# Kernel tuning notes

Measured on AMD Instinct MI355X. Metric: run time of the kernel, lower is better.

The kernel has to match this reference:

```python
import jax, jax.numpy as jnp
import numpy as np

HEAD_DIM = 128
NUM_Q_HEAD = 32
NUM_KV_HEAD = 8
WINDOW = 512
CAUSAL = True
SCALE = 1.0 / float(np.sqrt(HEAD_DIM))  # softmax_scale default 1/sqrt(d)
CAP = 30.0                               # softmax capping (temp ignored when cap is set)
CLIP_LO, CLIP_HI = -0.01, 1.01           # softmax clip range
NEG_INF = -1e30


def setup_inputs() -> dict:
    key = jax.random.key(0)
    kq, kk, kv = jax.random.split(key, 3)
    B, SQ, SK = 2, 2048, 2048
    q = jax.random.normal(kq, (B, SQ, NUM_Q_HEAD, HEAD_DIM), dtype=jnp.float32)
    k = jax.random.normal(kk, (B, SK, NUM_KV_HEAD, HEAD_DIM), dtype=jnp.float32)
    v = jax.random.normal(kv, (B, SK, NUM_KV_HEAD, HEAD_DIM), dtype=jnp.float32)
    return {"q": q, "k": k, "v": v}


def _sliding_window_mask(sq, sk):
    # query position i attends to kv position j with bottom-right alignment
    i = jnp.arange(sq)[:, None] + (sk - sq)  # [sq, 1]
    j = jnp.arange(sk)[None, :]              # [1, sk]
    allowed = j >= (i - WINDOW)
    if CAUSAL:
        allowed = allowed & (j <= i)
    else:
        allowed = allowed & (j <= i + WINDOW)
    return allowed  # [sq, sk] bool


def _attn(q, k, v):
    # q: [b, sq, hq, d]; k, v: [b, sk, hkv, d]
    B, SQ, HQ, D = q.shape
    SK = k.shape[1]
    groups = HQ // k.shape[2]
    k = jnp.repeat(k, groups, axis=2)  # GQA expand -> [b, sk, hq, d]
    v = jnp.repeat(v, groups, axis=2)

    logits = jnp.einsum('bqhd,bkhd->bhqk', q, k) * SCALE
    logits = CAP * jnp.tanh(logits / CAP)  # softmax capping

    allowed = _sliding_window_mask(SQ, SK)  # [sq, sk]
    logits = jnp.where(allowed[None, None], logits, NEG_INF)

    p = jax.nn.softmax(logits, axis=-1)
    # softmax clipping: clamp((hi-lo)*p + lo, 0, 1)
    p = jnp.clip((CLIP_HI - CLIP_LO) * p + CLIP_LO, 0.0, 1.0)

    out = jnp.einsum('bhqk,bkhd->bqhd', p, v)
    # rows with no allowed kv position -> zero output (torch code zeroes NaN rows)
    row_ok = jnp.any(allowed, axis=-1)  # [sq]
    out = jnp.where(row_ok[None, :, None, None], out, 0.0)
    return out


def reference(q, k, v):
    return _attn(q, k, v)
```

## Files before the change

### kernel.cpp

```cpp
#include <hip/hip_runtime.h>
#include <hip/hip_bf16.h>

#define B_    2
#define SQ_   2048
#define SK_   2048
#define HQ_   32
#define HKV_  8
#define D_    128
#define W_    512
#define KVT   64
#define MAXT  9

typedef short s16x8 __attribute__((ext_vector_type(8)));
typedef float f32x4 __attribute__((ext_vector_type(4)));

static __device__ __forceinline__ short bf16b(float x){
    __hip_bfloat16 h = __float2bfloat16(x);
    return *reinterpret_cast<short*>(&h);
}
static __device__ __forceinline__ float b2f(short u){
    return __uint_as_float(((unsigned)(unsigned short)u) << 16);
}
static __device__ __forceinline__ float fexp2(float x){ return __builtin_amdgcn_exp2f(x); }
static __device__ __forceinline__ unsigned pk2(float a, float b){
    return ((unsigned)(unsigned short)bf16b(a)) | (((unsigned)(unsigned short)bf16b(b)) << 16);
}

__global__ __launch_bounds__(512)
void attn_kernel(const float* __restrict__ q, const float* __restrict__ k,
                 const float* __restrict__ v, float* __restrict__ out){
    __shared__ short KV[KVT * D_];
    __shared__ short Pb[8 * 16 * KVT];

    int bid = blockIdx.x;
    int swz = (bid & 7) * 128 + (bid >> 3);
    int qt  = swz & 63;
    int hkv = (swz >> 6) & 7;
    int b   = swz >> 9;
    int qb  = qt * 32;

    int tid  = threadIdx.x;
    int w    = tid >> 6;
    int lane = tid & 63;
    int hl = w >> 1, qs = w & 1;
    int h  = hkv * 4 + hl;
    int qlo = qb + qs * 16;
    int g = lane >> 4, c = lane & 15;
    int qr = qlo + c;

    int t0 = qb >= 512 ? ((qb - 512) & ~63) : 0;
    int nt = (qb + 32 - t0 + 63) >> 6;

    s16x8 qf[4];
    {
        const float* qrow = q + (((size_t)b * SQ_ + qr) * HQ_ + h) * D_;
        #pragma unroll
        for (int db = 0; db < 4; ++db){
            float4 x = *(const float4*)(qrow + db * 32 + g * 8);
            float4 y = *(const float4*)(qrow + db * 32 + g * 8 + 4);
            s16x8 f;
            f[0]=bf16b(x.x); f[1]=bf16b(x.y); f[2]=bf16b(x.z); f[3]=bf16b(x.w);
            f[4]=bf16b(y.x); f[5]=bf16b(y.y); f[6]=bf16b(y.z); f[7]=bf16b(y.w);
            qf[db] = f;
        }
    }

    const float SCALE = 0.08838834764831845f;
    const float L2E   = 1.4426950408889634f;
    const float C1 = 2.0f * SCALE / 30.0f * L2E;
    const float C2 = -60.0f * L2E;
    const float C3 =  30.0f * L2E;

    int skrow = tid >> 3, sdg = tid & 7;
    int svp = tid & 31, svd = tid >> 5;
    const float* kbase = k + ((size_t)b * SK_ * HKV_ + hkv) * D_;
    const float* vbase = v + ((size_t)b * SK_ * HKV_ + hkv) * D_;

    float4 st[4];
    auto issueK = [&](int t){
        const float* p = kbase + (size_t)(t + skrow) * (HKV_ * D_) + sdg * 16;
        st[0] = *(const float4*)p;       st[1] = *(const float4*)(p + 4);
        st[2] = *(const float4*)(p + 8); st[3] = *(const float4*)(p + 12);
    };
    auto writeK = [&](){
        const float* f = (const float*)st;
        #pragma unroll
        for (int s = 0; s < 2; ++s){
            s16x8 o8;
            #pragma unroll
            for (int i = 0; i < 8; ++i) o8[i] = bf16b(f[s * 8 + i]);
            int byte = skrow * 256 + (((sdg * 32 + s * 16)) ^ ((skrow & 7) << 4));
            *(s16x8*)((char*)KV + byte) = o8;
        }
    };
    auto issueV = [&](int t){
        const float* p0 = vbase + (size_t)(t + 2 * svp) * (HKV_ * D_) + svd * 8;
        const float* p1 = p0 + HKV_ * D_;
        st[0] = *(const float4*)p0; st[1] = *(const float4*)(p0 + 4);
        st[2] = *(const float4*)p1; st[3] = *(const float4*)(p1 + 4);
    };
    auto writeV = [&](){
        const float* f = (const float*)st;
        #pragma unroll
        for (int i = 0; i < 8; ++i){
            int d = svd * 8 + i;
            unsigned wd = pk2(f[i], f[8 + i]);
            int byte = (d * 128 + svp * 4) ^ ((d & 7) << 4);
            *(unsigned*)((char*)KV + byte) = wd;
        }
    };

    float ls = 0.f;
    unsigned wv[MAXT][8];
    issueK(t0);
    #pragma unroll
    for (int ti = 0; ti < MAXT; ++ti){
        if (ti < nt){
            int t = t0 + ti * 64;
            __syncthreads();
            writeK();
            if (ti + 1 < nt) issueK(t0 + (ti + 1) * 64);
            __syncthreads();
            #pragma unroll
            for (int hh = 0; hh < 4; ++hh){
                int row = hh * 16 + c;
                f32x4 acc = {0.f, 0.f, 0.f, 0.f};
                #pragma unroll
                for (int db = 0; db < 4; ++db){
                    s16x8 kf = *(const s16x8*)((char*)KV + row * 256 + ((db * 64 + g * 16) ^ ((c & 7) << 4)));
                    acc = __builtin_amdgcn_mfma_f32_16x16x32_bf16(kf, qf[db], acc, 0, 0, 0);
                }
                int kvb = t + hh * 16 + 4 * g;
                float u[4];
                #pragma unroll
                for (int j = 0; j < 4; ++j){
                    float e = fexp2(acc[j] * C1);
                    float r = __builtin_amdgcn_rcpf(e + 1.0f);
                    float uu = fexp2(fmaf(r, C2, C3));
                    int kv = kvb + j;
                    bool ok = (kv <= qr) && (kv >= qr - W_);
                    u[j] = ok ? uu : 0.f;
                    ls += u[j];
                }
                wv[ti][hh * 2 + 0] = pk2(u[0], u[1]);
                wv[ti][hh * 2 + 1] = pk2(u[2], u[3]);
            }
        }
    }

    ls += __shfl_xor(ls, 16);
    ls += __shfl_xor(ls, 32);
    float rl = 1.02f / ls;

    f32x4 o[8];
    #pragma unroll
    for (int dt = 0; dt < 8; ++dt) o[dt] = (f32x4){0.f, 0.f, 0.f, 0.f};

    char* myPb = (char*)(Pb + w * 1024);

    issueV(t0);
    #pragma unroll
    for (int ti = 0; ti < MAXT; ++ti){
        if (ti < nt){
            __syncthreads();
            writeV();
            if (ti + 1 < nt) issueV(t0 + (ti + 1) * 64);
            __syncthreads();
            #pragma unroll
            for (int e = 0; e < 8; ++e){
                int hh = e >> 1, pr = e & 1;
                int byte = c * 128 + ((hh * 32 + g * 8 + pr * 4) ^ ((c & 7) << 4));
                *(unsigned*)(myPb + byte) = wv[ti][e];
            }
            asm volatile("s_waitcnt lgkmcnt(0)" ::: "memory");
            #pragma unroll
            for (int ks = 0; ks < 2; ++ks){
                s16x8 pa = *(const s16x8*)(myPb + c * 128 + ((ks * 64 + g * 16) ^ ((c & 7) << 4)));
                s16x8 pf;
                #pragma unroll
                for (int i = 0; i < 8; ++i){
                    float p = fmaf(b2f(pa[i]), rl, -0.01f);
                    p = fminf(fmaxf(p, 0.f), 1.f);
                    pf[i] = bf16b(p);
                }
                #pragma unroll
                for (int dt = 0; dt < 8; ++dt){
                    int d = dt * 16 + c;
                    s16x8 vf = *(const s16x8*)((char*)KV + d * 128 + ((ks * 64 + g * 16) ^ ((d & 7) << 4)));
                    o[dt] = __builtin_amdgcn_mfma_f32_16x16x32_bf16(pf, vf, o[dt], 0, 0, 0);
                }
            }
        }
    }

    float* ob = out + (((size_t)b * SQ_ + qlo) * HQ_ + h) * D_;
    #pragma unroll
    for (int dt = 0; dt < 8; ++dt){
        #pragma unroll
        for (int j = 0; j < 4; ++j){
            ob[(size_t)(4 * g + j) * (HQ_ * D_) + dt * 16 + c] = o[dt][j];
        }
    }
}

extern "C" void kernel_launch(void* const* d_in, const int* in_sizes, int n_in,
                              void* d_out, int out_size, void* d_ws, size_t ws_size,
                              hipStream_t stream){
    const float* q = (const float*)d_in[0];
    const float* k = (const float*)d_in[1];
    const float* v = (const float*)d_in[2];
    float* out = (float*)d_out;

    attn_kernel<<<B_ * HKV_ * (SQ_ / 32), 512, 0, stream>>>(q, k, v, out);
}
```

Measured before the change: 226.5 us.

## Pre-cast K/V to bf16, split KV tile across waves, double-buffer LDS

Adds a pre-pass that converts K and V to bf16 in workspace, so the attention kernel reads half the bytes and skips per-tile conversion. Each block now covers 16 query rows instead of 32. The 8 waves are split as 4 heads by 2 KV halves, with the row sums and partial outputs combined through shared memory at the end. K/V tiles are double-buffered with one barrier per tile, the XOR swizzles are changed, and setprio and sched_barrier hints are added. The cost is two extra kernel launches, a full pass over K/V, and twice as many blocks, each of which reloads K/V.

```diff
diff --git a/kernel.cpp b/kernel.cpp
--- a/kernel.cpp
+++ b/kernel.cpp
@@ -26,30 +26,39 @@
     return ((unsigned)(unsigned short)bf16b(a)) | (((unsigned)(unsigned short)bf16b(b)) << 16);
 }
 
-__global__ __launch_bounds__(512)
-void attn_kernel(const float* __restrict__ q, const float* __restrict__ k,
-                 const float* __restrict__ v, float* __restrict__ out){
-    __shared__ short KV[KVT * D_];
-    __shared__ short Pb[8 * 16 * KVT];
+__global__ void cast_bf16(const float* __restrict__ src, short* __restrict__ dst){
+    int idx = blockIdx.x * 256 + threadIdx.x;
+    const float4* p = reinterpret_cast<const float4*>(src) + (size_t)idx * 2;
+    float4 a = p[0], b = p[1];
+    s16x8 o;
+    o[0]=bf16b(a.x); o[1]=bf16b(a.y); o[2]=bf16b(a.z); o[3]=bf16b(a.w);
+    o[4]=bf16b(b.x); o[5]=bf16b(b.y); o[6]=bf16b(b.z); o[7]=bf16b(b.w);
+    reinterpret_cast<s16x8*>(dst)[idx] = o;
+}
+
+__global__ __launch_bounds__(512, 4)
+void attn_kernel(const float* __restrict__ q, const short* __restrict__ kb,
+                 const short* __restrict__ vb, float* __restrict__ out){
+    __shared__ short KVb[2][KVT * D_];
+    __shared__ short Pbb[8 * 16 * 32];
+    __shared__ float Ls[8][16];
 
     int bid = blockIdx.x;
-    int swz = (bid & 7) * 128 + (bid >> 3);
-    int qt  = swz & 63;
-    int hkv = (swz >> 6) & 7;
-    int b   = swz >> 9;
-    int qb  = qt * 32;
-
-    int tid  = threadIdx.x;
-    int w    = tid >> 6;
-    int lane = tid & 63;
-    int hl = w >> 1, qs = w & 1;
-    int h  = hkv * 4 + hl;
-    int qlo = qb + qs * 16;
+    int swz = (bid & 7) * 256 + (bid >> 3);
+    int qt  = swz & 127;
+    int hkv = (swz >> 7) & 7;
+    int b   = swz >> 10;
+    int qb  = qt * 16;
+
+    int tid = threadIdx.x;
+    int w = tid >> 6, lane = tid & 63;
+    int hl = w & 3, s = w >> 2;
+    int h = hkv * 4 + hl;
     int g = lane >> 4, c = lane & 15;
-    int qr = qlo + c;
+    int qr = qb + c;
 
     int t0 = qb >= 512 ? ((qb - 512) & ~63) : 0;
-    int nt = (qb + 32 - t0 + 63) >> 6;
+    int nt = (qb + 16 - t0 + 63) >> 6;
 
     s16x8 qf[4];
     {
@@ -71,135 +80,149 @@
     const float C2 = -60.0f * L2E;
     const float C3 =  30.0f * L2E;
 
-    int skrow = tid >> 3, sdg = tid & 7;
+    int skr = tid >> 3, sdg = tid & 7;
     int svp = tid & 31, svd = tid >> 5;
-    const float* kbase = k + ((size_t)b * SK_ * HKV_ + hkv) * D_;
-    const float* vbase = v + ((size_t)b * SK_ * HKV_ + hkv) * D_;
-
-    float4 st[4];
+    const short* kbase = kb + ((size_t)b * SK_ * HKV_ + hkv) * D_;
+    const short* vbase = vb + ((size_t)b * SK_ * HKV_ + hkv) * D_;
+
+    s16x8 st16[2];
     auto issueK = [&](int t){
-        const float* p = kbase + (size_t)(t + skrow) * (HKV_ * D_) + sdg * 16;
-        st[0] = *(const float4*)p;       st[1] = *(const float4*)(p + 4);
-        st[2] = *(const float4*)(p + 8); st[3] = *(const float4*)(p + 12);
-    };
-    auto writeK = [&](){
-        const float* f = (const float*)st;
-        #pragma unroll
-        for (int s = 0; s < 2; ++s){
-            s16x8 o8;
-            #pragma unroll
-            for (int i = 0; i < 8; ++i) o8[i] = bf16b(f[s * 8 + i]);
-            int byte = skrow * 256 + (((sdg * 32 + s * 16)) ^ ((skrow & 7) << 4));
-            *(s16x8*)((char*)KV + byte) = o8;
+        const short* p = kbase + (size_t)(t + skr) * (HKV_ * D_) + sdg * 16;
+        st16[0] = *(const s16x8*)p;
+        st16[1] = *(const s16x8*)(p + 8);
+    };
+    auto writeK = [&](short* buf){
+        #pragma unroll
+        for (int s2 = 0; s2 < 2; ++s2){
+            int byte = skr * 256 + (((2 * sdg + s2) ^ (skr & 15)) << 4);
+            *(s16x8*)((char*)buf + byte) = st16[s2];
         }
     };
     auto issueV = [&](int t){
-        const float* p0 = vbase + (size_t)(t + 2 * svp) * (HKV_ * D_) + svd * 8;
-        const float* p1 = p0 + HKV_ * D_;
-        st[0] = *(const float4*)p0; st[1] = *(const float4*)(p0 + 4);
-        st[2] = *(const float4*)p1; st[3] = *(const float4*)(p1 + 4);
-    };
-    auto writeV = [&](){
-        const float* f = (const float*)st;
+        const short* p0 = vbase + (size_t)(t + 2 * svp) * (HKV_ * D_) + svd * 8;
+        st16[0] = *(const s16x8*)p0;
+        st16[1] = *(const s16x8*)(p0 + HKV_ * D_);
+    };
+    auto writeV = [&](short* buf){
         #pragma unroll
         for (int i = 0; i < 8; ++i){
             int d = svd * 8 + i;
-            unsigned wd = pk2(f[i], f[8 + i]);
-            int byte = (d * 128 + svp * 4) ^ ((d & 7) << 4);
-            *(unsigned*)((char*)KV + byte) = wd;
+            unsigned wd = ((unsigned)(unsigned short)st16[0][i]) |
+                          (((unsigned)(unsigned short)st16[1][i]) << 16);
+            int byte = d * 128 + ((svp ^ (i << 2)) << 2);
+            *(unsigned*)((char*)buf + byte) = wd;
         }
     };
 
     float ls = 0.f;
-    unsigned wv[MAXT][8];
+    unsigned wv[MAXT][4];
     issueK(t0);
+    writeK(KVb[0]);
+    __syncthreads();
     #pragma unroll
     for (int ti = 0; ti < MAXT; ++ti){
         if (ti < nt){
             int t = t0 + ti * 64;
-            __syncthreads();
-            writeK();
+            const short* buf = KVb[ti & 1];
             if (ti + 1 < nt) issueK(t0 + (ti + 1) * 64);
-            __syncthreads();
-            #pragma unroll
-            for (int hh = 0; hh < 4; ++hh){
-                int row = hh * 16 + c;
+            #pragma unroll
+            for (int kvb = 0; kvb < 2; ++kvb){
+                int row = s * 32 + kvb * 16 + c;
                 f32x4 acc = {0.f, 0.f, 0.f, 0.f};
+                __builtin_amdgcn_s_setprio(1);
                 #pragma unroll
                 for (int db = 0; db < 4; ++db){
-                    s16x8 kf = *(const s16x8*)((char*)KV + row * 256 + ((db * 64 + g * 16) ^ ((c & 7) << 4)));
+                    s16x8 kf = *(const s16x8*)((char*)buf + row * 256 + (((db * 4 + g) ^ c) << 4));
                     acc = __builtin_amdgcn_mfma_f32_16x16x32_bf16(kf, qf[db], acc, 0, 0, 0);
                 }
-                int kvb = t + hh * 16 + 4 * g;
+                __builtin_amdgcn_s_setprio(0);
+                int kvb0 = t + s * 32 + kvb * 16 + 4 * g;
                 float u[4];
                 #pragma unroll
                 for (int j = 0; j < 4; ++j){
                     float e = fexp2(acc[j] * C1);
                     float r = __builtin_amdgcn_rcpf(e + 1.0f);
                     float uu = fexp2(fmaf(r, C2, C3));
-                    int kv = kvb + j;
+                    int kv = kvb0 + j;
                     bool ok = (kv <= qr) && (kv >= qr - W_);
                     u[j] = ok ? uu : 0.f;
                     ls += u[j];
                 }
-                wv[ti][hh * 2 + 0] = pk2(u[0], u[1]);
-                wv[ti][hh * 2 + 1] = pk2(u[2], u[3]);
-            }
+                wv[ti][kvb * 2 + 0] = pk2(u[0], u[1]);
+                wv[ti][kvb * 2 + 1] = pk2(u[2], u[3]);
+            }
+            if (ti + 1 < nt){ writeK(KVb[(ti + 1) & 1]); __syncthreads(); }
         }
     }
 
     ls += __shfl_xor(ls, 16);
     ls += __shfl_xor(ls, 32);
-    float rl = 1.02f / ls;
+    if (lane < 16) Ls[w][lane] = ls;
+    issueV(t0);
+    __syncthreads();
+    float rl = 1.02f / (Ls[hl][c] + Ls[hl + 4][c]);
 
     f32x4 o[8];
     #pragma unroll
     for (int dt = 0; dt < 8; ++dt) o[dt] = (f32x4){0.f, 0.f, 0.f, 0.f};
 
-    char* myPb = (char*)(Pb + w * 1024);
-
-    issueV(t0);
+    char* myPb = (char*)Pbb + w * 1024;
+    int q2 = (c >> 1) & 3;
+
+    writeV(KVb[0]);
+    __syncthreads();
     #pragma unroll
     for (int ti = 0; ti < MAXT; ++ti){
         if (ti < nt){
-            __syncthreads();
-            writeV();
+            const short* buf = KVb[ti & 1];
             if (ti + 1 < nt) issueV(t0 + (ti + 1) * 64);
-            __syncthreads();
-            #pragma unroll
-            for (int e = 0; e < 8; ++e){
-                int hh = e >> 1, pr = e & 1;
-                int byte = c * 128 + ((hh * 32 + g * 8 + pr * 4) ^ ((c & 7) << 4));
+            #pragma unroll
+            for (int e = 0; e < 4; ++e){
+                int kvb = e >> 1, pr = e & 1;
+                int byte = c * 64 + (((kvb * 2 + (g >> 1)) ^ q2) << 4) + (g & 1) * 8 + pr * 4;
                 *(unsigned*)(myPb + byte) = wv[ti][e];
             }
             asm volatile("s_waitcnt lgkmcnt(0)" ::: "memory");
-            #pragma unroll
-            for (int ks = 0; ks < 2; ++ks){
-                s16x8 pa = *(const s16x8*)(myPb + c * 128 + ((ks * 64 + g * 16) ^ ((c & 7) << 4)));
-                s16x8 pf;
-                #pragma unroll
-                for (int i = 0; i < 8; ++i){
-                    float p = fmaf(b2f(pa[i]), rl, -0.01f);
-                    p = fminf(fmaxf(p, 0.f), 1.f);
-                    pf[i] = bf16b(p);
-                }
-                #pragma unroll
-                for (int dt = 0; dt < 8; ++dt){
-                    int d = dt * 16 + c;
-                    s16x8 vf = *(const s16x8*)((char*)KV + d * 128 + ((ks * 64 + g * 16) ^ ((d & 7) << 4)));
-                    o[dt] = __builtin_amdgcn_mfma_f32_16x16x32_bf16(pf, vf, o[dt], 0, 0, 0);
-                }
-            }
-        }
-    }
-
-    float* ob = out + (((size_t)b * SQ_ + qlo) * HQ_ + h) * D_;
-    #pragma unroll
-    for (int dt = 0; dt < 8; ++dt){
-        #pragma unroll
-        for (int j = 0; j < 4; ++j){
-            ob[(size_t)(4 * g + j) * (HQ_ * D_) + dt * 16 + c] = o[dt][j];
-        }
+            __builtin_amdgcn_sched_barrier(0);
+            s16x8 pa = *(const s16x8*)(myPb + c * 64 + ((g ^ q2) << 4));
+            s16x8 pf;
+            #pragma unroll
+            for (int i = 0; i < 8; ++i){
+                float p = fmaf(b2f(pa[i]), rl, -0.01f);
+                p = fminf(fmaxf(p, 0.f), 1.f);
+                pf[i] = bf16b(p);
+            }
+            __builtin_amdgcn_s_setprio(1);
+            #pragma unroll
+            for (int dt = 0; dt < 8; ++dt){
+                int d = dt * 16 + c;
+                s16x8 vf = *(const s16x8*)((char*)buf + d * 128 + (((s * 4 + g) ^ (c & 7)) << 4));
+                o[dt] = __builtin_amdgcn_mfma_f32_16x16x32_bf16(pf, vf, o[dt], 0, 0, 0);
+            }
+            __builtin_amdgcn_s_setprio(0);
+            if (ti + 1 < nt){ writeV(KVb[(ti + 1) & 1]); __syncthreads(); }
+        }
+    }
+
+    __syncthreads();
+    float* Ob = (float*)KVb;
+    if (s == 1){
+        #pragma unroll
+        for (int dt = 0; dt < 8; ++dt)
+            #pragma unroll
+            for (int j = 0; j < 4; ++j)
+                Ob[hl * 2048 + (dt * 4 + j) * 64 + lane] = o[dt][j];
+    }
+    __syncthreads();
+    if (s == 0){
+        float* ob = out + (((size_t)b * SQ_ + qb) * HQ_ + h) * D_;
+        #pragma unroll
+        for (int dt = 0; dt < 8; ++dt)
+            #pragma unroll
+            for (int j = 0; j < 4; ++j){
+                float r2 = o[dt][j] + Ob[hl * 2048 + (dt * 4 + j) * 64 + lane];
+                ob[(size_t)(4 * g + j) * (HQ_ * D_) + dt * 16 + c] = r2;
+            }
     }
 }
 
@@ -211,5 +234,10 @@
     const float* v = (const float*)d_in[2];
     float* out = (float*)d_out;
 
-    attn_kernel<<<B_ * HKV_ * (SQ_ / 32), 512, 0, stream>>>(q, k, v, out);
-}
+    short* kbp = (short*)d_ws;
+    short* vbp = (short*)d_ws + 4194304;
+
+    cast_bf16<<<2048, 256, 0, stream>>>(k, kbp);
+    cast_bf16<<<2048, 256, 0, stream>>>(v, vbp);
+    attn_kernel<<<B_ * HKV_ * (SQ_ / 16), 512, 0, stream>>>(q, kbp, vbp, out);
+}
```

New measurement: 208.5 us. 8.0% less time.
